# Kernel tuning notes

Hardware: AMD Instinct MI355X
Metric: run time of the kernel (lower is better)

## Reference

```python
import jax, jax.numpy as jnp
import numpy as np

D_MODEL = 768
D_INNER = 1536      # expand=2
D_STATE = 16
DT_RANK = 48        # ceil(768/16)
D_CONV = 4
DEPTH = 24
NUM_CLASSES = 527
GRID = (8, 64)      # (128/16, 1024/16)
SEQ = GRID[0] * GRID[1]
TOKPOS = SEQ // 2   # middle cls token position


def setup_inputs() -> dict:
    key = jax.random.key(0)
    ks = jax.random.split(key, 12)
    rn = lambda k, s, sc=0.02: jax.random.normal(k, s, jnp.float32) * sc
    A_init = jnp.log(jnp.arange(1, D_STATE + 1, dtype=jnp.float32))  # S4D-real init
    return {
        "x": jax.random.normal(ks[0], (1, 1, 128, 1024), jnp.float32),
        "patch_w": rn(ks[1], (D_MODEL, 1, 16, 16)),
        "patch_b": jnp.zeros((D_MODEL,), jnp.float32),
        "cls_token": rn(ks[2], (1, 1, D_MODEL)),
        "pos_embed": rn(ks[3], (1, SEQ + 1, D_MODEL)),
        "in_proj_w": rn(ks[4], (DEPTH, 2 * D_INNER, D_MODEL)),
        "conv_w": rn(ks[5], (DEPTH, 2, D_INNER, D_CONV), 0.1),
        "conv_b": jnp.zeros((DEPTH, 2, D_INNER), jnp.float32),
        "xproj_w": rn(ks[6], (DEPTH, 2, DT_RANK + 2 * D_STATE, D_INNER)),
        "dtproj_w": rn(ks[7], (DEPTH, 2, D_INNER, DT_RANK), 0.1),
        "dtproj_b": jnp.full((DEPTH, 2, D_INNER), float(np.log(np.expm1(0.01))), jnp.float32),
        "A_log": jnp.ones((DEPTH, 2, D_INNER, 1), jnp.float32) * A_init,
        "D_skip": jnp.ones((DEPTH, 2, D_INNER), jnp.float32),
        "out_proj_w": rn(ks[8], (DEPTH, D_MODEL, D_INNER)),
        "norm_w": jnp.ones((DEPTH, D_MODEL), jnp.float32),
        "norm_f_w": jnp.ones((D_MODEL,), jnp.float32),
        "head_w": rn(ks[9], (NUM_CLASSES, D_MODEL)),
        "head_b": jnp.zeros((NUM_CLASSES,), jnp.float32),
    }


def _rmsnorm(x, w, eps=1e-5):
    return x * jax.lax.rsqrt(jnp.mean(x * x, axis=-1, keepdims=True) + eps) * w


def _causal_conv_silu(x, w, b):
    # x [B,d,L], depthwise causal conv, kernel D_CONV, left-pad D_CONV-1
    L = x.shape[-1]
    xp = jnp.pad(x, ((0, 0), (0, 0), (D_CONV - 1, 0)))
    y = sum(w[:, k, None] * xp[:, :, k:k + L] for k in range(D_CONV)) + b[:, None]
    return jax.nn.silu(y)


def _selective_scan(dt, A, Bm, C, u):
    # dt,u: [B,d,L]; Bm,C: [B,N,L]; A: [d,N] (negative)
    def step(h, inp):
        dt_t, B_t, C_t, u_t = inp           # [B,d],[B,N],[B,N],[B,d]
        h = h * jnp.exp(dt_t[..., None] * A) + (dt_t * u_t)[..., None] * B_t[:, None, :]
        return h, jnp.einsum('bdn,bn->bd', h, C_t)
    h0 = jnp.zeros((dt.shape[0], A.shape[0], A.shape[1]), dt.dtype)
    mv = lambda a: jnp.moveaxis(a, -1, 0)
    _, ys = jax.lax.scan(step, h0, (mv(dt), mv(Bm), mv(C), mv(u)))
    return jnp.moveaxis(ys, 0, -1)          # [B,d,L]


def _mamba_dir(x, z, cw, cb, xw, dw, db, A_log, Dsk):
    xc = _causal_conv_silu(x, cw, cb)
    dbl = jnp.einsum('bdl,cd->bcl', xc, xw)                 # [B, R+2N, L]
    dt = jax.nn.softplus(jnp.einsum('brl,dr->bdl', dbl[:, :DT_RANK], dw) + db[:, None])
    Bm = dbl[:, DT_RANK:DT_RANK + D_STATE]
    C = dbl[:, DT_RANK + D_STATE:]
    y = _selective_scan(dt, -jnp.exp(A_log), Bm, C, xc) + Dsk[:, None] * xc
    return y * jax.nn.silu(z)


def _block(carry, p):
    hidden, residual = carry
    ipw, cw, cb, xw, dw, db, A_log, Dsk, opw, nw = p
    residual = residual + hidden                            # add -> norm -> mixer
    h = _rmsnorm(residual, nw)
    xz = jnp.einsum('bld,ed->ble', h, ipw)                  # [B,L,2*d_inner]
    x, z = jnp.split(jnp.moveaxis(xz, -1, 1), 2, axis=1)    # each [B,d_inner,L]
    yf = _mamba_dir(x, z, cw[0], cb[0], xw[0], dw[0], db[0], A_log[0], Dsk[0])
    yb = _mamba_dir(x[:, :, ::-1], z[:, :, ::-1], cw[1], cb[1], xw[1], dw[1],
                    db[1], A_log[1], Dsk[1])[:, :, ::-1]
    out = jnp.einsum('bdl,ed->ble', (yf + yb) * 0.5, opw)   # if_devide_out
    return (out, residual), None


def reference(x, patch_w, patch_b, cls_token, pos_embed, in_proj_w, conv_w, conv_b,
              xproj_w, dtproj_w, dtproj_b, A_log, D_skip, out_proj_w, norm_w,
              norm_f_w, head_w, head_b):
    h = jax.lax.conv_general_dilated(x, patch_w, (16, 16), 'VALID',
                                     dimension_numbers=('NCHW', 'OIHW', 'NCHW'))
    h = h + patch_b[None, :, None, None]
    B = h.shape[0]
    h = h.reshape(B, D_MODEL, SEQ).transpose(0, 2, 1)       # [B,512,768]
    cls = jnp.broadcast_to(cls_token, (B, 1, D_MODEL))
    h = jnp.concatenate([h[:, :TOKPOS], cls, h[:, TOKPOS:]], axis=1)  # [B,513,768]
    h = h + pos_embed
    carry = (h, jnp.zeros_like(h))
    (hidden, residual), _ = jax.lax.scan(
        _block, carry,
        (in_proj_w, conv_w, conv_b, xproj_w, dtproj_w, dtproj_b, A_log, D_skip,
         out_proj_w, norm_w))
    out = _rmsnorm(residual + hidden, norm_f_w)
    feat = out[:, TOKPOS]                                   # middle cls token
    return feat @ head_w.T + head_b
```

## Files before the change

### kernel.cpp

```cpp
#include <hip/hip_runtime.h>

#define L_SEQ 513
#define DM 768
#define DI 1536
#define DSTATE 16
#define DTRANK 48
#define NCLS 527
#define DEPTH 24
#define NC 32
#define CLEN 17

typedef unsigned short u16;
typedef __bf16 bf16x8 __attribute__((ext_vector_type(8)));
typedef float f32x4 __attribute__((ext_vector_type(4)));

#define MFMA_BF16(A, B, C) __builtin_amdgcn_mfma_f32_16x16x32_bf16(A, B, C, 0, 0, 0)

__device__ inline u16 f2bf(float x) {
  unsigned u = __float_as_uint(x);
  return (u16)((u + 0x7FFFu + ((u >> 16) & 1u)) >> 16);
}
__device__ inline float bf2f(u16 h) { return __uint_as_float((unsigned)h << 16); }
__device__ inline void split2(float v, u16& h, u16& l) {
  h = f2bf(v);
  l = f2bf(v - bf2f(h));
}

__global__ void wconvert_kernel(const float* __restrict__ src,
                                u16* __restrict__ hi, u16* __restrict__ lo,
                                long n4) {
  long i = (long)blockIdx.x * 256 + threadIdx.x;
  long stride = (long)gridDim.x * 256;
  for (; i < n4; i += stride) {
    float4 v = ((const float4*)src)[i];
    ushort4 h, l;
    split2(v.x, h.x, l.x);
    split2(v.y, h.y, l.y);
    split2(v.z, h.z, l.z);
    split2(v.w, h.w, l.w);
    ((ushort4*)hi)[i] = h;
    ((ushort4*)lo)[i] = l;
  }
}

__global__ void patch_embed_kernel(const float* __restrict__ x,
                                   const float* __restrict__ pw,
                                   const float* __restrict__ pb,
                                   const float* __restrict__ cls,
                                   const float* __restrict__ pos,
                                   float* __restrict__ hidden,
                                   float* __restrict__ residual) {
  int c = blockIdx.x * 256 + threadIdx.x;
  int s = blockIdx.y;
  if (c >= DM) return;
  float val;
  if (s == 256) {
    val = cls[c];
  } else {
    int p = s - (s > 256 ? 1 : 0);
    int gy = p >> 6, gx = p & 63;
    const float* xp = x + gy * 16 * 1024 + gx * 16;
    const float* wp = pw + c * 256;
    float acc = pb[c];
#pragma unroll 4
    for (int ky = 0; ky < 16; ++ky)
#pragma unroll
      for (int kx = 0; kx < 16; ++kx)
        acc += xp[ky * 1024 + kx] * wp[ky * 16 + kx];
    val = acc;
  }
  long idx = (long)s * DM + c;
  hidden[idx] = val + pos[idx];
  residual[idx] = 0.f;
}

__global__ void rmsnorm_kernel(const float* __restrict__ hidden,
                               float* __restrict__ residual,
                               u16* __restrict__ hnh, u16* __restrict__ hnl,
                               const float* __restrict__ w) {
  int t = blockIdx.x;
  const float* hrow = hidden + (long)t * DM;
  float* rrow = residual + (long)t * DM;
  int tid = threadIdx.x;
  float vals[3];
  float ss = 0.f;
#pragma unroll
  for (int i = 0; i < 3; ++i) {
    int c = tid + i * 256;
    float v = rrow[c] + hrow[c];
    vals[i] = v;
    rrow[c] = v;
    ss += v * v;
  }
#pragma unroll
  for (int o = 32; o; o >>= 1) ss += __shfl_down(ss, o, 64);
  __shared__ float sacc[4];
  if ((tid & 63) == 0) sacc[tid >> 6] = ss;
  __syncthreads();
  float tot = sacc[0] + sacc[1] + sacc[2] + sacc[3];
  float rs = rsqrtf(tot / (float)DM + 1e-5f);
#pragma unroll
  for (int i = 0; i < 3; ++i) {
    int c = tid + i * 256;
    float y = vals[i] * rs * w[c];
    u16 h, l;
    split2(y, h, l);
    hnh[(long)t * DM + c] = h;
    hnl[(long)t * DM + c] = l;
  }
}

__global__ __launch_bounds__(256) void gemm_hl(
    const u16* __restrict__ Ah, const u16* __restrict__ Al,
    const u16* __restrict__ Bh, const u16* __restrict__ Bl,
    float* __restrict__ C,
    int M, int N, int K, int lda, int ldb, int ldc,
    long sA, long sB, long sC,
    const float* __restrict__ bias, long sBias, int act,
    u16* __restrict__ Chi, u16* __restrict__ Clo, int ncap, int ldhl, long sChl) {
  int bz = blockIdx.z;
  const u16* Ahb = Ah + (long)bz * sA;
  const u16* Alb = Al + (long)bz * sA;
  const u16* Bhb = Bh + (long)bz * sB;
  const u16* Blb = Bl + (long)bz * sB;
  float* Cb = C + (long)bz * sC;
  const float* biasb = bias ? bias + (long)bz * sBias : nullptr;

  __shared__ u16 AhS[2][64 * 32], AlS[2][64 * 32];
  __shared__ u16 BhS[2][64 * 32], BlS[2][64 * 32];

  int tid = threadIdx.x;
  int m0 = blockIdx.y * 64, n0 = blockIdx.x * 64;

  int srow = tid >> 2;
  int sg = tid & 3;
  int sIdx = srow * 32 + ((sg ^ ((srow >> 1) & 3)) << 3);
  int arow = m0 + srow, brow = n0 + srow;
  const u16* ah_p = Ahb + (long)arow * lda + sg * 8;
  const u16* al_p = Alb + (long)arow * lda + sg * 8;
  const u16* bh_p = Bhb + (long)brow * ldb + sg * 8;
  const u16* bl_p = Blb + (long)brow * ldb + sg * 8;
  bool aok = arow < M, bok = brow < N;

  int lane = tid & 63;
  int w = tid >> 6;
  int wr = w >> 1, wc = w & 1;
  int fr = lane & 15, kh = lane >> 4;
  int rowA0 = wr * 32 + fr, rowA1 = rowA0 + 16;
  int rowB0 = wc * 32 + fr, rowB1 = rowB0 + 16;
  int offA0 = rowA0 * 32 + ((kh ^ ((rowA0 >> 1) & 3)) << 3);
  int offA1 = rowA1 * 32 + ((kh ^ ((rowA1 >> 1) & 3)) << 3);
  int offB0 = rowB0 * 32 + ((kh ^ ((rowB0 >> 1) & 3)) << 3);
  int offB1 = rowB1 * 32 + ((kh ^ ((rowB1 >> 1) & 3)) << 3);

  f32x4 acc00 = {0.f, 0.f, 0.f, 0.f}, acc01 = {0.f, 0.f, 0.f, 0.f};
  f32x4 acc10 = {0.f, 0.f, 0.f, 0.f}, acc11 = {0.f, 0.f, 0.f, 0.f};

  int nst = (K + 31) / 32;
  int kg = sg * 8;

  uint4 ra, rl_, rb, rbl;
  {
    uint4 z = {0, 0, 0, 0};
    ra = (aok && kg + 8 <= K) ? *(const uint4*)ah_p : z;
    rl_ = (aok && kg + 8 <= K) ? *(const uint4*)al_p : z;
    rb = (bok && kg + 8 <= K) ? *(const uint4*)bh_p : z;
    rbl = (bok && kg + 8 <= K) ? *(const uint4*)bl_p : z;
  }
  *(uint4*)&AhS[0][sIdx] = ra;
  *(uint4*)&AlS[0][sIdx] = rl_;
  *(uint4*)&BhS[0][sIdx] = rb;
  *(uint4*)&BlS[0][sIdx] = rbl;

  for (int s = 0; s < nst; ++s) {
    if (s + 1 < nst) {
      int kb = (s + 1) * 32;
      uint4 z = {0, 0, 0, 0};
      bool kok = kb + kg + 8 <= K;
      ra = (aok && kok) ? *(const uint4*)(ah_p + kb) : z;
      rl_ = (aok && kok) ? *(const uint4*)(al_p + kb) : z;
      rb = (bok && kok) ? *(const uint4*)(bh_p + kb) : z;
      rbl = (bok && kok) ? *(const uint4*)(bl_p + kb) : z;
    }
    __syncthreads();
    int b = s & 1;

    bf16x8 ah0 = __builtin_bit_cast(bf16x8, *(const uint4*)&AhS[b][offA0]);
    bf16x8 ah1 = __builtin_bit_cast(bf16x8, *(const uint4*)&AhS[b][offA1]);
    bf16x8 al0 = __builtin_bit_cast(bf16x8, *(const uint4*)&AlS[b][offA0]);
    bf16x8 al1 = __builtin_bit_cast(bf16x8, *(const uint4*)&AlS[b][offA1]);
    bf16x8 bh0 = __builtin_bit_cast(bf16x8, *(const uint4*)&BhS[b][offB0]);
    bf16x8 bh1 = __builtin_bit_cast(bf16x8, *(const uint4*)&BhS[b][offB1]);
    bf16x8 bl0 = __builtin_bit_cast(bf16x8, *(const uint4*)&BlS[b][offB0]);
    bf16x8 bl1 = __builtin_bit_cast(bf16x8, *(const uint4*)&BlS[b][offB1]);

    acc00 = MFMA_BF16(ah0, bh0, acc00);
    acc00 = MFMA_BF16(ah0, bl0, acc00);
    acc00 = MFMA_BF16(al0, bh0, acc00);
    acc01 = MFMA_BF16(ah0, bh1, acc01);
    acc01 = MFMA_BF16(ah0, bl1, acc01);
    acc01 = MFMA_BF16(al0, bh1, acc01);
    acc10 = MFMA_BF16(ah1, bh0, acc10);
    acc10 = MFMA_BF16(ah1, bl0, acc10);
    acc10 = MFMA_BF16(al1, bh0, acc10);
    acc11 = MFMA_BF16(ah1, bh1, acc11);
    acc11 = MFMA_BF16(ah1, bl1, acc11);
    acc11 = MFMA_BF16(al1, bh1, acc11);

    if (s + 1 < nst) {
      int b2 = (s + 1) & 1;
      *(uint4*)&AhS[b2][sIdx] = ra;
      *(uint4*)&AlS[b2][sIdx] = rl_;
      *(uint4*)&BhS[b2][sIdx] = rb;
      *(uint4*)&BlS[b2][sIdx] = rbl;
    }
  }

  u16* Chib = Chi ? Chi + (long)bz * sChl : nullptr;
  u16* Clob = Clo ? Clo + (long)bz * sChl : nullptr;
  int mbase = m0 + wr * 32, nbase = n0 + wc * 32;
#define WRITE_FRAG(ACC, MI, NI)                                       \
  {                                                                   \
    int n = nbase + (NI)*16 + fr;                                     \
    if (n < N) {                                                      \
      float bv = biasb ? biasb[n] : 0.f;                              \
      _Pragma("unroll")                                               \
      for (int r = 0; r < 4; ++r) {                                   \
        int m = mbase + (MI)*16 + kh * 4 + r;                         \
        if (m < M) {                                                  \
          float v = ACC[r] + bv;                                      \
          if (act == 1) v = (v > 20.f) ? v : log1pf(__expf(v));       \
          Cb[(long)m * ldc + n] = v;                                  \
          if (Chib && n < ncap) {                                     \
            u16 hh, ll;                                               \
            split2(v, hh, ll);                                        \
            Chib[(long)m * ldhl + n] = hh;                            \
            Clob[(long)m * ldhl + n] = ll;                            \
          }                                                           \
        }                                                             \
      }                                                               \
    }                                                                 \
  }
  WRITE_FRAG(acc00, 0, 0)
  WRITE_FRAG(acc01, 0, 1)
  WRITE_FRAG(acc10, 1, 0)
  WRITE_FRAG(acc11, 1, 1)
#undef WRITE_FRAG
}

__global__ void conv_silu_kernel(const float* __restrict__ xz,
                                 const float* __restrict__ cw,
                                 const float* __restrict__ cb,
                                 float* __restrict__ xc,
                                 u16* __restrict__ xch, u16* __restrict__ xcl) {
  int dir = blockIdx.y;
  int idx = blockIdx.x * 256 + threadIdx.x;
  int d = idx % DI;
  int t = idx / DI;
  const float* w = cw + ((long)dir * DI + d) * 4;
  float acc = cb[dir * DI + d];
#pragma unroll
  for (int k = 0; k < 4; ++k) {
    int tau = t + k - 3;
    if (tau >= 0) {
      int tsrc = dir ? (L_SEQ - 1 - tau) : tau;
      acc += w[k] * xz[(long)tsrc * (2 * DI) + d];
    }
  }
  float s = acc / (1.f + __expf(-acc));
  long o = ((long)dir * L_SEQ + t) * DI + d;
  xc[o] = s;
  u16 h, l;
  split2(s, h, l);
  xch[o] = h;
  xcl[o] = l;
}

__global__ __launch_bounds__(256) void scan_part1(
    const float* __restrict__ dtv_arr,
    const float* __restrict__ xc,
    const float* __restrict__ dbl,
    const float* __restrict__ A_log,
    float* __restrict__ part_h,
    float* __restrict__ part_S) {
  int dir = blockIdx.z;
  int c = blockIdx.y;
  int d = blockIdx.x * 256 + threadIdx.x;
  int t0 = c * CLEN;
  int t1 = min(t0 + CLEN, L_SEQ);

  __shared__ float Bs[CLEN][DSTATE];
  const float* dblp = dbl + (long)dir * L_SEQ * 80;
  for (int i = threadIdx.x; i < (t1 - t0) * DSTATE; i += 256) {
    int tt = i >> 4, n = i & 15;
    Bs[tt][n] = dblp[(long)(t0 + tt) * 80 + DTRANK + n];
  }
  __syncthreads();

  float negA[DSTATE], h[DSTATE];
#pragma unroll
  for (int n = 0; n < DSTATE; ++n) {
    negA[n] = -__expf(A_log[((long)dir * DI + d) * DSTATE + n]);
    h[n] = 0.f;
  }
  const float* dtp = dtv_arr + (long)dir * L_SEQ * DI;
  const float* xcp = xc + (long)dir * L_SEQ * DI;

  float S = 0.f;
  float dt_c = 0.f, u_c = 0.f;
  if (t0 < t1) {
    dt_c = dtp[(long)t0 * DI + d];
    u_c = xcp[(long)t0 * DI + d];
  }
  for (int t = t0; t < t1; ++t) {
    float dt_n = 0.f, u_n = 0.f;
    if (t + 1 < t1) {
      dt_n = dtp[(long)(t + 1) * DI + d];
      u_n = xcp[(long)(t + 1) * DI + d];
    }
    S += dt_c;
    float du = dt_c * u_c;
    int tt = t - t0;
#pragma unroll
    for (int n = 0; n < DSTATE; ++n)
      h[n] = h[n] * __expf(dt_c * negA[n]) + du * Bs[tt][n];
    dt_c = dt_n;
    u_c = u_n;
  }
  long base = ((long)dir * NC + c) * DI + d;
  part_S[base] = S;
#pragma unroll
  for (int n = 0; n < DSTATE; ++n) part_h[base * DSTATE + n] = h[n];
}

__global__ void scan_fix(const float* __restrict__ A_log,
                         const float* __restrict__ part_S,
                         float* __restrict__ part_h) {
  int idx = blockIdx.x * 256 + threadIdx.x;
  int n = idx & 15;
  int d = (idx >> 4) % DI;
  int dir = (idx >> 4) / DI;
  float negA = -__expf(A_log[((long)dir * DI + d) * DSTATE + n]);
  float h = 0.f;
  for (int c = 0; c < NC; ++c) {
    long base = ((long)dir * NC + c) * DI + d;
    float S = part_S[base];
    float q = part_h[base * DSTATE + n];
    part_h[base * DSTATE + n] = h;
    h = h * __expf(negA * S) + q;
  }
}

__global__ __launch_bounds__(256) void scan_part2(
    const float* __restrict__ dtv_arr,
    const float* __restrict__ xc,
    const float* __restrict__ dbl,
    const float* __restrict__ xz,
    const float* __restrict__ A_log,
    const float* __restrict__ Dsk,
    const float* __restrict__ part_h,
    float* __restrict__ y) {
  int dir = blockIdx.z;
  int c = blockIdx.y;
  int d = blockIdx.x * 256 + threadIdx.x;
  int t0 = c * CLEN;
  int t1 = min(t0 + CLEN, L_SEQ);

  __shared__ float Bs[CLEN][DSTATE];
  __shared__ float Cs[CLEN][DSTATE];
  const float* dblp = dbl + (long)dir * L_SEQ * 80;
  for (int i = threadIdx.x; i < (t1 - t0) * 2 * DSTATE; i += 256) {
    int tt = i >> 5, j = i & 31;
    float v = dblp[(long)(t0 + tt) * 80 + DTRANK + j];
    if (j < DSTATE) Bs[tt][j] = v; else Cs[tt][j - DSTATE] = v;
  }
  __syncthreads();

  float negA[DSTATE], h[DSTATE];
  long base = ((long)dir * NC + c) * DI + d;
#pragma unroll
  for (int n = 0; n < DSTATE; ++n) {
    negA[n] = -__expf(A_log[((long)dir * DI + d) * DSTATE + n]);
    h[n] = part_h[base * DSTATE + n];
  }
  float dskip = Dsk[dir * DI + d];
  const float* dtp = dtv_arr + (long)dir * L_SEQ * DI;
  const float* xcp = xc + (long)dir * L_SEQ * DI;

  float dt_c = 0.f, u_c = 0.f;
  if (t0 < t1) {
    dt_c = dtp[(long)t0 * DI + d];
    u_c = xcp[(long)t0 * DI + d];
  }
  for (int t = t0; t < t1; ++t) {
    float dt_n = 0.f, u_n = 0.f;
    if (t + 1 < t1) {
      dt_n = dtp[(long)(t + 1) * DI + d];
      u_n = xcp[(long)(t + 1) * DI + d];
    }
    float du = dt_c * u_c;
    int tt = t - t0;
    float acc = 0.f;
#pragma unroll
    for (int n = 0; n < DSTATE; ++n) {
      h[n] = h[n] * __expf(dt_c * negA[n]) + du * Bs[tt][n];
      acc += h[n] * Cs[tt][n];
    }
    int tsrc = dir ? (L_SEQ - 1 - t) : t;
    float zv = xz[(long)tsrc * (2 * DI) + DI + d];
    float sz = zv / (1.f + __expf(-zv));
    y[((long)dir * L_SEQ + tsrc) * DI + d] = (acc + dskip * u_c) * sz;
    dt_c = dt_n;
    u_c = u_n;
  }
}

__global__ void yavg_kernel(const float* __restrict__ yf,
                            const float* __restrict__ yb,
                            u16* __restrict__ yh, u16* __restrict__ yl) {
  long i = (long)blockIdx.x * 256 + threadIdx.x;
  if (i >= (long)L_SEQ * DI / 4) return;
  float4 a = ((const float4*)yf)[i];
  float4 b = ((const float4*)yb)[i];
  ushort4 h, l;
  split2(0.5f * (a.x + b.x), h.x, l.x);
  split2(0.5f * (a.y + b.y), h.y, l.y);
  split2(0.5f * (a.z + b.z), h.z, l.z);
  split2(0.5f * (a.w + b.w), h.w, l.w);
  ((ushort4*)yh)[i] = h;
  ((ushort4*)yl)[i] = l;
}

__global__ void head_kernel(const float* __restrict__ residual,
                            const float* __restrict__ hidden,
                            const float* __restrict__ nfw,
                            const float* __restrict__ hw,
                            const float* __restrict__ hb,
                            float* __restrict__ out) {
  int j = blockIdx.x;
  int tid = threadIdx.x;
  const float* r = residual + (long)256 * DM;
  const float* h = hidden + (long)256 * DM;
  float ss = 0.f, dp = 0.f;
#pragma unroll
  for (int i = 0; i < 3; ++i) {
    int c = tid + i * 256;
    float v = r[c] + h[c];
    ss += v * v;
    dp += v * nfw[c] * hw[(long)j * DM + c];
  }
#pragma unroll
  for (int o = 32; o; o >>= 1) {
    ss += __shfl_down(ss, o, 64);
    dp += __shfl_down(dp, o, 64);
  }
  __shared__ float s1[4], s2[4];
  if ((tid & 63) == 0) {
    s1[tid >> 6] = ss;
    s2[tid >> 6] = dp;
  }
  __syncthreads();
  if (tid == 0) {
    float tot = s1[0] + s1[1] + s1[2] + s1[3];
    float d = s2[0] + s2[1] + s2[2] + s2[3];
    out[j] = d * rsqrtf(tot / (float)DM + 1e-5f) + hb[j];
  }
}

extern "C" void kernel_launch(void* const* d_in, const int* in_sizes, int n_in,
                              void* d_out, int out_size, void* d_ws, size_t ws_size,
                              hipStream_t stream) {
  const float* x        = (const float*)d_in[0];
  const float* patch_w  = (const float*)d_in[1];
  const float* patch_b  = (const float*)d_in[2];
  const float* cls_tok  = (const float*)d_in[3];
  const float* pos_emb  = (const float*)d_in[4];
  const float* in_proj  = (const float*)d_in[5];
  const float* conv_w   = (const float*)d_in[6];
  const float* conv_b   = (const float*)d_in[7];
  const float* xproj_w  = (const float*)d_in[8];
  const float* dtproj_w = (const float*)d_in[9];
  const float* dtproj_b = (const float*)d_in[10];
  const float* A_log    = (const float*)d_in[11];
  const float* D_skip   = (const float*)d_in[12];
  const float* out_proj = (const float*)d_in[13];
  const float* norm_w   = (const float*)d_in[14];
  const float* norm_f_w = (const float*)d_in[15];
  const float* head_w   = (const float*)d_in[16];
  const float* head_b   = (const float*)d_in[17];
  float* out = (float*)d_out;

  float* ws = (float*)d_ws;
  float* residual = ws; ws += (long)L_SEQ * DM;
  float* hidden   = ws; ws += (long)L_SEQ * DM;
  float* xz       = ws; ws += (long)L_SEQ * 2 * DI;
  float* xc       = ws; ws += (long)2 * L_SEQ * DI;
  float* dbl      = ws; ws += (long)2 * L_SEQ * 80;
  float* dtb      = ws; ws += (long)2 * L_SEQ * DI;
  float* yb       = ws; ws += (long)2 * L_SEQ * DI;
  float* part_h   = ws; ws += (long)2 * NC * DI * DSTATE;
  float* part_S   = ws; ws += (long)2 * NC * DI;

  u16* wsu = (u16*)ws;
  const long N_HN  = (long)L_SEQ * DM;
  const long N_XC  = (long)2 * L_SEQ * DI;
  const long N_D48 = (long)2 * L_SEQ * DTRANK;
  const long N_YA  = (long)L_SEQ * DI;
  const long N_WI  = (long)DEPTH * 2 * DI * DM;
  const long N_WX  = (long)DEPTH * 2 * 80 * DI;
  const long N_WD  = (long)DEPTH * 2 * DI * DTRANK;
  const long N_WO  = (long)DEPTH * DM * DI;
  u16* hn_h  = wsu; wsu += N_HN;
  u16* hn_l  = wsu; wsu += N_HN;
  u16* xc_h  = wsu; wsu += N_XC;
  u16* xc_l  = wsu; wsu += N_XC;
  u16* d48_h = wsu; wsu += N_D48;
  u16* d48_l = wsu; wsu += N_D48;
  u16* ya_h  = wsu; wsu += N_YA;
  u16* ya_l  = wsu; wsu += N_YA;
  u16* wi_h  = wsu; wsu += N_WI;
  u16* wi_l  = wsu; wsu += N_WI;
  u16* wx_h  = wsu; wsu += N_WX;
  u16* wx_l  = wsu; wsu += N_WX;
  u16* wd_h  = wsu; wsu += N_WD;
  u16* wd_l  = wsu; wsu += N_WD;
  u16* wo_h  = wsu; wsu += N_WO;
  u16* wo_l  = wsu; wsu += N_WO;

  wconvert_kernel<<<2048, 256, 0, stream>>>(in_proj,  wi_h, wi_l, N_WI / 4);
  wconvert_kernel<<<512,  256, 0, stream>>>(xproj_w,  wx_h, wx_l, N_WX / 4);
  wconvert_kernel<<<512,  256, 0, stream>>>(dtproj_w, wd_h, wd_l, N_WD / 4);
  wconvert_kernel<<<2048, 256, 0, stream>>>(out_proj, wo_h, wo_l, N_WO / 4);

  patch_embed_kernel<<<dim3(3, L_SEQ), 256, 0, stream>>>(
      x, patch_w, patch_b, cls_tok, pos_emb, hidden, residual);

  for (int l = 0; l < DEPTH; ++l) {
    const u16* wih = wi_h + (long)l * 2 * DI * DM;
    const u16* wil = wi_l + (long)l * 2 * DI * DM;
    const u16* wxh = wx_h + (long)l * 2 * 80 * DI;
    const u16* wxl = wx_l + (long)l * 2 * 80 * DI;
    const u16* wdh = wd_h + (long)l * 2 * DI * DTRANK;
    const u16* wdl = wd_l + (long)l * 2 * DI * DTRANK;
    const u16* woh = wo_h + (long)l * DM * DI;
    const u16* wol = wo_l + (long)l * DM * DI;
    const float* cw  = conv_w   + (long)l * 2 * DI * 4;
    const float* cb  = conv_b   + (long)l * 2 * DI;
    const float* db  = dtproj_b + (long)l * 2 * DI;
    const float* Al  = A_log    + (long)l * 2 * DI * DSTATE;
    const float* Dk  = D_skip   + (long)l * 2 * DI;
    const float* nw  = norm_w   + (long)l * DM;

    rmsnorm_kernel<<<L_SEQ, 256, 0, stream>>>(hidden, residual, hn_h, hn_l, nw);

    gemm_hl<<<dim3(48, 9, 1), 256, 0, stream>>>(
        hn_h, hn_l, wih, wil, xz, L_SEQ, 2 * DI, DM, DM, DM, 2 * DI, 0, 0, 0,
        nullptr, 0, 0, nullptr, nullptr, 0, 0, 0);

    conv_silu_kernel<<<dim3(3078, 2), 256, 0, stream>>>(xz, cw, cb, xc, xc_h, xc_l);

    gemm_hl<<<dim3(2, 9, 2), 256, 0, stream>>>(
        xc_h, xc_l, wxh, wxl, dbl, L_SEQ, 80, DI, DI, DI, 80,
        (long)L_SEQ * DI, (long)80 * DI, (long)L_SEQ * 80,
        nullptr, 0, 0, d48_h, d48_l, DTRANK, DTRANK, (long)L_SEQ * DTRANK);

    gemm_hl<<<dim3(24, 9, 2), 256, 0, stream>>>(
        d48_h, d48_l, wdh, wdl, dtb, L_SEQ, DI, DTRANK, DTRANK, DTRANK, DI,
        (long)L_SEQ * DTRANK, (long)DI * DTRANK, (long)L_SEQ * DI,
        db, DI, 1, nullptr, nullptr, 0, 0, 0);

    scan_part1<<<dim3(DI / 256, NC, 2), 256, 0, stream>>>(
        dtb, xc, dbl, Al, part_h, part_S);
    scan_fix<<<(2 * DI * DSTATE) / 256, 256, 0, stream>>>(Al, part_S, part_h);
    scan_part2<<<dim3(DI / 256, NC, 2), 256, 0, stream>>>(
        dtb, xc, dbl, xz, Al, Dk, part_h, yb);

    yavg_kernel<<<(L_SEQ * DI / 4 + 255) / 256, 256, 0, stream>>>(
        yb, yb + (long)L_SEQ * DI, ya_h, ya_l);

    gemm_hl<<<dim3(12, 9, 1), 256, 0, stream>>>(
        ya_h, ya_l, woh, wol, hidden, L_SEQ, DM, DI, DI, DI, DM, 0, 0, 0,
        nullptr, 0, 0, nullptr, nullptr, 0, 0, 0);
  }

  head_kernel<<<NCLS, 256, 0, stream>>>(residual, hidden, norm_f_w, head_w, head_b, out);
}
```

Before: 3.969 ms.

## Use 128x128 split-K GEMM tiles and fuse the three-pass scan into one kernel

Replaces the 64x64 hi/lo bf16 GEMM with a 128x128-tile version that supports split-K. Partial sums are written to separate buffers and reduced by the consumers: rmsnorm, conv_silu, a new xreduce kernel and the head. The chunked selective scan's three kernels (part1, fix, part2) are merged into one block-local kernel that does the chunk carry fix-up in shared memory. This aims to raise MFMA reuse and occupancy on the small-M GEMMs and to cut launch and global round-trip costs for the scan. The cost is extra partial-sum traffic and reduction reads, and fewer threads for the scan's sequential passes.

```diff
diff --git a/kernel.cpp b/kernel.cpp
--- a/kernel.cpp
+++ b/kernel.cpp
@@ -9,6 +9,9 @@
 #define DEPTH 24
 #define NC 32
 #define CLEN 17
+#define SKI 3
+#define SKX 8
+#define SKO 8
 
 typedef unsigned short u16;
 typedef __bf16 bf16x8 __attribute__((ext_vector_type(8)));
@@ -24,6 +27,10 @@
 __device__ inline void split2(float v, u16& h, u16& l) {
   h = f2bf(v);
   l = f2bf(v - bf2f(h));
+}
+__device__ __forceinline__ int lofs(int row, int g) {
+  int swz = (row & 3) ^ ((row >> 2) & 3);
+  return row * 32 + ((g ^ swz) << 3);
 }
 
 __global__ void wconvert_kernel(const float* __restrict__ src,
@@ -74,12 +81,11 @@
   residual[idx] = 0.f;
 }
 
-__global__ void rmsnorm_kernel(const float* __restrict__ hidden,
+__global__ void rmsnorm_kernel(const float* __restrict__ hp, int nparts, long pstr,
                                float* __restrict__ residual,
                                u16* __restrict__ hnh, u16* __restrict__ hnl,
                                const float* __restrict__ w) {
   int t = blockIdx.x;
-  const float* hrow = hidden + (long)t * DM;
   float* rrow = residual + (long)t * DM;
   int tid = threadIdx.x;
   float vals[3];
@@ -87,7 +93,8 @@
 #pragma unroll
   for (int i = 0; i < 3; ++i) {
     int c = tid + i * 256;
-    float v = rrow[c] + hrow[c];
+    float v = rrow[c];
+    for (int p = 0; p < nparts; ++p) v += hp[(long)p * pstr + (long)t * DM + c];
     vals[i] = v;
     rrow[c] = v;
     ss += v * v;
@@ -110,149 +117,132 @@
   }
 }
 
-__global__ __launch_bounds__(256) void gemm_hl(
+#define LOADSTEP(KB)                                                    \
+  {                                                                     \
+    int k_ = (KB) + g0 * 8;                                             \
+    bool kk_ = (k_ + 8 <= kend);                                        \
+    uint4 zz = {0, 0, 0, 0};                                            \
+    a0h = (kk_ && am0) ? *(const uint4*)(Ahb + aoff0 + k_) : zz;        \
+    a1h = (kk_ && am1) ? *(const uint4*)(Ahb + aoff1 + k_) : zz;        \
+    a0l = (kk_ && am0) ? *(const uint4*)(Alb + aoff0 + k_) : zz;        \
+    a1l = (kk_ && am1) ? *(const uint4*)(Alb + aoff1 + k_) : zz;        \
+    b0h = (kk_ && bm0) ? *(const uint4*)(Bhb + boff0 + k_) : zz;        \
+    b1h = (kk_ && bm1) ? *(const uint4*)(Bhb + boff1 + k_) : zz;        \
+    b0l = (kk_ && bm0) ? *(const uint4*)(Blb + boff0 + k_) : zz;        \
+    b1l = (kk_ && bm1) ? *(const uint4*)(Blb + boff1 + k_) : zz;        \
+  }
+#define WRITEBUF(B)                        \
+  {                                        \
+    *(uint4*)&SA[B][0][l0] = a0h;          \
+    *(uint4*)&SA[B][0][l1] = a1h;          \
+    *(uint4*)&SA[B][1][l0] = a0l;          \
+    *(uint4*)&SA[B][1][l1] = a1l;          \
+    *(uint4*)&SB[B][0][l0] = b0h;          \
+    *(uint4*)&SB[B][0][l1] = b1h;          \
+    *(uint4*)&SB[B][1][l0] = b0l;          \
+    *(uint4*)&SB[B][1][l1] = b1l;          \
+  }
+
+__global__ __launch_bounds__(256) void gemm128(
     const u16* __restrict__ Ah, const u16* __restrict__ Al,
     const u16* __restrict__ Bh, const u16* __restrict__ Bl,
     float* __restrict__ C,
     int M, int N, int K, int lda, int ldb, int ldc,
     long sA, long sB, long sC,
-    const float* __restrict__ bias, long sBias, int act,
-    u16* __restrict__ Chi, u16* __restrict__ Clo, int ncap, int ldhl, long sChl) {
-  int bz = blockIdx.z;
-  const u16* Ahb = Ah + (long)bz * sA;
-  const u16* Alb = Al + (long)bz * sA;
-  const u16* Bhb = Bh + (long)bz * sB;
-  const u16* Blb = Bl + (long)bz * sB;
-  float* Cb = C + (long)bz * sC;
-  const float* biasb = bias ? bias + (long)bz * sBias : nullptr;
-
-  __shared__ u16 AhS[2][64 * 32], AlS[2][64 * 32];
-  __shared__ u16 BhS[2][64 * 32], BlS[2][64 * 32];
+    int NSK, int Kb, long sP,
+    const float* __restrict__ bias, long sBias, int act) {
+  int z = blockIdx.z;
+  int batch = z / NSK, sk = z - batch * NSK;
+  const u16* Ahb = Ah + (long)batch * sA;
+  const u16* Alb = Al + (long)batch * sA;
+  const u16* Bhb = Bh + (long)batch * sB;
+  const u16* Blb = Bl + (long)batch * sB;
+  float* Cb = C + (long)batch * sC + (long)sk * sP;
+  const float* biasb = bias ? bias + (long)batch * sBias : nullptr;
+  int ks0 = sk * Kb;
+  int kend = min(ks0 + Kb, K);
+
+  __shared__ u16 SA[2][2][128 * 32];
+  __shared__ u16 SB[2][2][128 * 32];
 
   int tid = threadIdx.x;
-  int m0 = blockIdx.y * 64, n0 = blockIdx.x * 64;
-
-  int srow = tid >> 2;
-  int sg = tid & 3;
-  int sIdx = srow * 32 + ((sg ^ ((srow >> 1) & 3)) << 3);
-  int arow = m0 + srow, brow = n0 + srow;
-  const u16* ah_p = Ahb + (long)arow * lda + sg * 8;
-  const u16* al_p = Alb + (long)arow * lda + sg * 8;
-  const u16* bh_p = Bhb + (long)brow * ldb + sg * 8;
-  const u16* bl_p = Blb + (long)brow * ldb + sg * 8;
-  bool aok = arow < M, bok = brow < N;
-
-  int lane = tid & 63;
-  int w = tid >> 6;
+  int m0 = blockIdx.y * 128, n0 = blockIdx.x * 128;
+
+  int r0 = tid >> 2, g0 = tid & 3;
+  int r1 = r0 + 64;
+  int l0 = lofs(r0, g0), l1 = lofs(r1, g0);
+  long aoff0 = (long)(m0 + r0) * lda, aoff1 = (long)(m0 + r1) * lda;
+  long boff0 = (long)(n0 + r0) * ldb, boff1 = (long)(n0 + r1) * ldb;
+  bool am0 = (m0 + r0) < M, am1 = (m0 + r1) < M;
+  bool bm0 = (n0 + r0) < N, bm1 = (n0 + r1) < N;
+
+  int lane = tid & 63, w = tid >> 6;
   int wr = w >> 1, wc = w & 1;
   int fr = lane & 15, kh = lane >> 4;
-  int rowA0 = wr * 32 + fr, rowA1 = rowA0 + 16;
-  int rowB0 = wc * 32 + fr, rowB1 = rowB0 + 16;
-  int offA0 = rowA0 * 32 + ((kh ^ ((rowA0 >> 1) & 3)) << 3);
-  int offA1 = rowA1 * 32 + ((kh ^ ((rowA1 >> 1) & 3)) << 3);
-  int offB0 = rowB0 * 32 + ((kh ^ ((rowB0 >> 1) & 3)) << 3);
-  int offB1 = rowB1 * 32 + ((kh ^ ((rowB1 >> 1) & 3)) << 3);
-
-  f32x4 acc00 = {0.f, 0.f, 0.f, 0.f}, acc01 = {0.f, 0.f, 0.f, 0.f};
-  f32x4 acc10 = {0.f, 0.f, 0.f, 0.f}, acc11 = {0.f, 0.f, 0.f, 0.f};
-
-  int nst = (K + 31) / 32;
-  int kg = sg * 8;
-
-  uint4 ra, rl_, rb, rbl;
-  {
-    uint4 z = {0, 0, 0, 0};
-    ra = (aok && kg + 8 <= K) ? *(const uint4*)ah_p : z;
-    rl_ = (aok && kg + 8 <= K) ? *(const uint4*)al_p : z;
-    rb = (bok && kg + 8 <= K) ? *(const uint4*)bh_p : z;
-    rbl = (bok && kg + 8 <= K) ? *(const uint4*)bl_p : z;
-  }
-  *(uint4*)&AhS[0][sIdx] = ra;
-  *(uint4*)&AlS[0][sIdx] = rl_;
-  *(uint4*)&BhS[0][sIdx] = rb;
-  *(uint4*)&BlS[0][sIdx] = rbl;
+  int offA[4], offB[4];
+#pragma unroll
+  for (int i = 0; i < 4; ++i) {
+    offA[i] = lofs(wr * 64 + i * 16 + fr, kh);
+    offB[i] = lofs(wc * 64 + i * 16 + fr, kh);
+  }
+
+  f32x4 acc[4][4] = {};
+  int nst = (kend - ks0 + 31) >> 5;
+  uint4 a0h, a1h, a0l, a1l, b0h, b1h, b0l, b1l;
+  LOADSTEP(ks0);
+  WRITEBUF(0);
+  if (nst > 1) LOADSTEP(ks0 + 32);
+  __syncthreads();
 
   for (int s = 0; s < nst; ++s) {
+    int b = s & 1;
+    bf16x8 fah[4], fal[4], fbh[4], fbl[4];
+#pragma unroll
+    for (int i = 0; i < 4; ++i) {
+      fah[i] = __builtin_bit_cast(bf16x8, *(const uint4*)&SA[b][0][offA[i]]);
+      fal[i] = __builtin_bit_cast(bf16x8, *(const uint4*)&SA[b][1][offA[i]]);
+      fbh[i] = __builtin_bit_cast(bf16x8, *(const uint4*)&SB[b][0][offB[i]]);
+      fbl[i] = __builtin_bit_cast(bf16x8, *(const uint4*)&SB[b][1][offB[i]]);
+    }
+#pragma unroll
+    for (int mi = 0; mi < 4; ++mi)
+#pragma unroll
+      for (int ni = 0; ni < 4; ++ni) {
+        acc[mi][ni] = MFMA_BF16(fah[mi], fbh[ni], acc[mi][ni]);
+        acc[mi][ni] = MFMA_BF16(fah[mi], fbl[ni], acc[mi][ni]);
+        acc[mi][ni] = MFMA_BF16(fal[mi], fbh[ni], acc[mi][ni]);
+      }
     if (s + 1 < nst) {
-      int kb = (s + 1) * 32;
-      uint4 z = {0, 0, 0, 0};
-      bool kok = kb + kg + 8 <= K;
-      ra = (aok && kok) ? *(const uint4*)(ah_p + kb) : z;
-      rl_ = (aok && kok) ? *(const uint4*)(al_p + kb) : z;
-      rb = (bok && kok) ? *(const uint4*)(bh_p + kb) : z;
-      rbl = (bok && kok) ? *(const uint4*)(bl_p + kb) : z;
+      WRITEBUF(b ^ 1);
+      if (s + 2 < nst) LOADSTEP(ks0 + (s + 2) * 32);
     }
     __syncthreads();
-    int b = s & 1;
-
-    bf16x8 ah0 = __builtin_bit_cast(bf16x8, *(const uint4*)&AhS[b][offA0]);
-    bf16x8 ah1 = __builtin_bit_cast(bf16x8, *(const uint4*)&AhS[b][offA1]);
-    bf16x8 al0 = __builtin_bit_cast(bf16x8, *(const uint4*)&AlS[b][offA0]);
-    bf16x8 al1 = __builtin_bit_cast(bf16x8, *(const uint4*)&AlS[b][offA1]);
-    bf16x8 bh0 = __builtin_bit_cast(bf16x8, *(const uint4*)&BhS[b][offB0]);
-    bf16x8 bh1 = __builtin_bit_cast(bf16x8, *(const uint4*)&BhS[b][offB1]);
-    bf16x8 bl0 = __builtin_bit_cast(bf16x8, *(const uint4*)&BlS[b][offB0]);
-    bf16x8 bl1 = __builtin_bit_cast(bf16x8, *(const uint4*)&BlS[b][offB1]);
-
-    acc00 = MFMA_BF16(ah0, bh0, acc00);
-    acc00 = MFMA_BF16(ah0, bl0, acc00);
-    acc00 = MFMA_BF16(al0, bh0, acc00);
-    acc01 = MFMA_BF16(ah0, bh1, acc01);
-    acc01 = MFMA_BF16(ah0, bl1, acc01);
-    acc01 = MFMA_BF16(al0, bh1, acc01);
-    acc10 = MFMA_BF16(ah1, bh0, acc10);
-    acc10 = MFMA_BF16(ah1, bl0, acc10);
-    acc10 = MFMA_BF16(al1, bh0, acc10);
-    acc11 = MFMA_BF16(ah1, bh1, acc11);
-    acc11 = MFMA_BF16(ah1, bl1, acc11);
-    acc11 = MFMA_BF16(al1, bh1, acc11);
-
-    if (s + 1 < nst) {
-      int b2 = (s + 1) & 1;
-      *(uint4*)&AhS[b2][sIdx] = ra;
-      *(uint4*)&AlS[b2][sIdx] = rl_;
-      *(uint4*)&BhS[b2][sIdx] = rb;
-      *(uint4*)&BlS[b2][sIdx] = rbl;
-    }
-  }
-
-  u16* Chib = Chi ? Chi + (long)bz * sChl : nullptr;
-  u16* Clob = Clo ? Clo + (long)bz * sChl : nullptr;
-  int mbase = m0 + wr * 32, nbase = n0 + wc * 32;
-#define WRITE_FRAG(ACC, MI, NI)                                       \
-  {                                                                   \
-    int n = nbase + (NI)*16 + fr;                                     \
-    if (n < N) {                                                      \
-      float bv = biasb ? biasb[n] : 0.f;                              \
-      _Pragma("unroll")                                               \
-      for (int r = 0; r < 4; ++r) {                                   \
-        int m = mbase + (MI)*16 + kh * 4 + r;                         \
-        if (m < M) {                                                  \
-          float v = ACC[r] + bv;                                      \
-          if (act == 1) v = (v > 20.f) ? v : log1pf(__expf(v));       \
-          Cb[(long)m * ldc + n] = v;                                  \
-          if (Chib && n < ncap) {                                     \
-            u16 hh, ll;                                               \
-            split2(v, hh, ll);                                        \
-            Chib[(long)m * ldhl + n] = hh;                            \
-            Clob[(long)m * ldhl + n] = ll;                            \
-          }                                                           \
-        }                                                             \
-      }                                                               \
-    }                                                                 \
-  }
-  WRITE_FRAG(acc00, 0, 0)
-  WRITE_FRAG(acc01, 0, 1)
-  WRITE_FRAG(acc10, 1, 0)
-  WRITE_FRAG(acc11, 1, 1)
-#undef WRITE_FRAG
-}
-
-__global__ void conv_silu_kernel(const float* __restrict__ xz,
+  }
+
+#pragma unroll
+  for (int mi = 0; mi < 4; ++mi)
+#pragma unroll
+    for (int ni = 0; ni < 4; ++ni) {
+      int n = n0 + wc * 64 + ni * 16 + fr;
+      if (n >= N) continue;
+      float bv = biasb ? biasb[n] : 0.f;
+#pragma unroll
+      for (int r = 0; r < 4; ++r) {
+        int m = m0 + wr * 64 + mi * 16 + kh * 4 + r;
+        if (m >= M) continue;
+        float v = acc[mi][ni][r] + bv;
+        if (act == 1) v = (v > 20.f) ? v : log1pf(__expf(v));
+        Cb[(long)m * ldc + n] = v;
+      }
+    }
+}
+
+__global__ void conv_silu_kernel(const float* __restrict__ xz_p,
                                  const float* __restrict__ cw,
                                  const float* __restrict__ cb,
                                  float* __restrict__ xc,
                                  u16* __restrict__ xch, u16* __restrict__ xcl) {
+  const long PZ = (long)L_SEQ * 2 * DI;
   int dir = blockIdx.y;
   int idx = blockIdx.x * 256 + threadIdx.x;
   int d = idx % DI;
@@ -264,7 +254,9 @@
     int tau = t + k - 3;
     if (tau >= 0) {
       int tsrc = dir ? (L_SEQ - 1 - tau) : tau;
-      acc += w[k] * xz[(long)tsrc * (2 * DI) + d];
+      long o = (long)tsrc * (2 * DI) + d;
+      float xv = xz_p[o] + xz_p[o + PZ] + xz_p[o + 2 * PZ];
+      acc += w[k] * xv;
     }
   }
   float s = acc / (1.f + __expf(-acc));
@@ -276,142 +268,120 @@
   xcl[o] = l;
 }
 
-__global__ __launch_bounds__(256) void scan_part1(
+__global__ void xreduce_kernel(const float* __restrict__ dbl_p,
+                               float* __restrict__ dbl,
+                               u16* __restrict__ d48h, u16* __restrict__ d48l) {
+  int idx = blockIdx.x * 256 + threadIdx.x;
+  if (idx >= 2 * L_SEQ * 80) return;
+  int j = idx % 80;
+  int td = idx / 80;
+  int dir = td / L_SEQ;
+  int t = td - dir * L_SEQ;
+  const float* p = dbl_p + (long)dir * SKX * L_SEQ * 80 + (long)t * 80 + j;
+  float v = 0.f;
+#pragma unroll
+  for (int q = 0; q < SKX; ++q) v += p[(long)q * L_SEQ * 80];
+  dbl[((long)dir * L_SEQ + t) * 80 + j] = v;
+  if (j < DTRANK) {
+    u16 h, l;
+    split2(v, h, l);
+    long o = ((long)dir * L_SEQ + t) * DTRANK + j;
+    d48h[o] = h;
+    d48l[o] = l;
+  }
+}
+
+__global__ __launch_bounds__(256) void scan_all(
     const float* __restrict__ dtv_arr,
     const float* __restrict__ xc,
     const float* __restrict__ dbl,
+    const float* __restrict__ xz_p,
     const float* __restrict__ A_log,
-    float* __restrict__ part_h,
-    float* __restrict__ part_S) {
-  int dir = blockIdx.z;
-  int c = blockIdx.y;
-  int d = blockIdx.x * 256 + threadIdx.x;
-  int t0 = c * CLEN;
-  int t1 = min(t0 + CLEN, L_SEQ);
-
-  __shared__ float Bs[CLEN][DSTATE];
-  const float* dblp = dbl + (long)dir * L_SEQ * 80;
-  for (int i = threadIdx.x; i < (t1 - t0) * DSTATE; i += 256) {
-    int tt = i >> 4, n = i & 15;
-    Bs[tt][n] = dblp[(long)(t0 + tt) * 80 + DTRANK + n];
-  }
-  __syncthreads();
-
-  float negA[DSTATE], h[DSTATE];
-#pragma unroll
-  for (int n = 0; n < DSTATE; ++n) {
-    negA[n] = -__expf(A_log[((long)dir * DI + d) * DSTATE + n]);
-    h[n] = 0.f;
-  }
+    const float* __restrict__ Dsk,
+    float* __restrict__ y) {
+  const long PZ = (long)L_SEQ * 2 * DI;
+  int dir = blockIdx.y;
+  int d0 = blockIdx.x * 8;
+  int tid = threadIdx.x;
+  __shared__ float Q[8][NC][DSTATE];
+  __shared__ float Sv[8][NC];
+
   const float* dtp = dtv_arr + (long)dir * L_SEQ * DI;
   const float* xcp = xc + (long)dir * L_SEQ * DI;
-
-  float S = 0.f;
-  float dt_c = 0.f, u_c = 0.f;
-  if (t0 < t1) {
-    dt_c = dtp[(long)t0 * DI + d];
-    u_c = xcp[(long)t0 * DI + d];
-  }
-  for (int t = t0; t < t1; ++t) {
-    float dt_n = 0.f, u_n = 0.f;
-    if (t + 1 < t1) {
-      dt_n = dtp[(long)(t + 1) * DI + d];
-      u_n = xcp[(long)(t + 1) * DI + d];
-    }
-    S += dt_c;
-    float du = dt_c * u_c;
-    int tt = t - t0;
-#pragma unroll
-    for (int n = 0; n < DSTATE; ++n)
-      h[n] = h[n] * __expf(dt_c * negA[n]) + du * Bs[tt][n];
-    dt_c = dt_n;
-    u_c = u_n;
-  }
-  long base = ((long)dir * NC + c) * DI + d;
-  part_S[base] = S;
-#pragma unroll
-  for (int n = 0; n < DSTATE; ++n) part_h[base * DSTATE + n] = h[n];
-}
-
-__global__ void scan_fix(const float* __restrict__ A_log,
-                         const float* __restrict__ part_S,
-                         float* __restrict__ part_h) {
-  int idx = blockIdx.x * 256 + threadIdx.x;
-  int n = idx & 15;
-  int d = (idx >> 4) % DI;
-  int dir = (idx >> 4) / DI;
-  float negA = -__expf(A_log[((long)dir * DI + d) * DSTATE + n]);
-  float h = 0.f;
-  for (int c = 0; c < NC; ++c) {
-    long base = ((long)dir * NC + c) * DI + d;
-    float S = part_S[base];
-    float q = part_h[base * DSTATE + n];
-    part_h[base * DSTATE + n] = h;
-    h = h * __expf(negA * S) + q;
-  }
-}
-
-__global__ __launch_bounds__(256) void scan_part2(
-    const float* __restrict__ dtv_arr,
-    const float* __restrict__ xc,
-    const float* __restrict__ dbl,
-    const float* __restrict__ xz,
-    const float* __restrict__ A_log,
-    const float* __restrict__ Dsk,
-    const float* __restrict__ part_h,
-    float* __restrict__ y) {
-  int dir = blockIdx.z;
-  int c = blockIdx.y;
-  int d = blockIdx.x * 256 + threadIdx.x;
-  int t0 = c * CLEN;
-  int t1 = min(t0 + CLEN, L_SEQ);
-
-  __shared__ float Bs[CLEN][DSTATE];
-  __shared__ float Cs[CLEN][DSTATE];
   const float* dblp = dbl + (long)dir * L_SEQ * 80;
-  for (int i = threadIdx.x; i < (t1 - t0) * 2 * DSTATE; i += 256) {
-    int tt = i >> 5, j = i & 31;
-    float v = dblp[(long)(t0 + tt) * 80 + DTRANK + j];
-    if (j < DSTATE) Bs[tt][j] = v; else Cs[tt][j - DSTATE] = v;
+
+  int dl = tid & 7, c = tid >> 3;
+  int d = d0 + dl;
+  float negA[DSTATE];
+#pragma unroll
+  for (int n = 0; n < DSTATE; ++n)
+    negA[n] = -__expf(A_log[((long)dir * DI + d) * DSTATE + n]);
+
+  int t0 = c * CLEN, t1 = min(t0 + CLEN, L_SEQ);
+  {
+    float h[DSTATE];
+#pragma unroll
+    for (int n = 0; n < DSTATE; ++n) h[n] = 0.f;
+    float S = 0.f;
+    for (int t = t0; t < t1; ++t) {
+      float dt = dtp[(long)t * DI + d];
+      float u = xcp[(long)t * DI + d];
+      float du = dt * u;
+      S += dt;
+      const float4* B4 = (const float4*)(dblp + (long)t * 80 + DTRANK);
+      float4 b0 = B4[0], b1 = B4[1], b2 = B4[2], b3 = B4[3];
+      float Bv[DSTATE] = {b0.x, b0.y, b0.z, b0.w, b1.x, b1.y, b1.z, b1.w,
+                          b2.x, b2.y, b2.z, b2.w, b3.x, b3.y, b3.z, b3.w};
+#pragma unroll
+      for (int n = 0; n < DSTATE; ++n)
+        h[n] = h[n] * __expf(dt * negA[n]) + du * Bv[n];
+    }
+    Sv[dl][c] = S;
+#pragma unroll
+    for (int n = 0; n < DSTATE; ++n) Q[dl][c][n] = h[n];
   }
   __syncthreads();
-
-  float negA[DSTATE], h[DSTATE];
-  long base = ((long)dir * NC + c) * DI + d;
-#pragma unroll
-  for (int n = 0; n < DSTATE; ++n) {
-    negA[n] = -__expf(A_log[((long)dir * DI + d) * DSTATE + n]);
-    h[n] = part_h[base * DSTATE + n];
-  }
-  float dskip = Dsk[dir * DI + d];
-  const float* dtp = dtv_arr + (long)dir * L_SEQ * DI;
-  const float* xcp = xc + (long)dir * L_SEQ * DI;
-
-  float dt_c = 0.f, u_c = 0.f;
-  if (t0 < t1) {
-    dt_c = dtp[(long)t0 * DI + d];
-    u_c = xcp[(long)t0 * DI + d];
-  }
-  for (int t = t0; t < t1; ++t) {
-    float dt_n = 0.f, u_n = 0.f;
-    if (t + 1 < t1) {
-      dt_n = dtp[(long)(t + 1) * DI + d];
-      u_n = xcp[(long)(t + 1) * DI + d];
-    }
-    float du = dt_c * u_c;
-    int tt = t - t0;
-    float acc = 0.f;
-#pragma unroll
-    for (int n = 0; n < DSTATE; ++n) {
-      h[n] = h[n] * __expf(dt_c * negA[n]) + du * Bs[tt][n];
-      acc += h[n] * Cs[tt][n];
-    }
-    int tsrc = dir ? (L_SEQ - 1 - t) : t;
-    float zv = xz[(long)tsrc * (2 * DI) + DI + d];
-    float sz = zv / (1.f + __expf(-zv));
-    y[((long)dir * L_SEQ + tsrc) * DI + d] = (acc + dskip * u_c) * sz;
-    dt_c = dt_n;
-    u_c = u_n;
+  if (tid < 128) {
+    int fdl = tid >> 4, n = tid & 15;
+    int fd = d0 + fdl;
+    float nA = -__expf(A_log[((long)dir * DI + fd) * DSTATE + n]);
+    float h = 0.f;
+    for (int cc = 0; cc < NC; ++cc) {
+      float S = Sv[fdl][cc];
+      float q = Q[fdl][cc][n];
+      Q[fdl][cc][n] = h;
+      h = h * __expf(nA * S) + q;
+    }
+  }
+  __syncthreads();
+  {
+    float h[DSTATE];
+#pragma unroll
+    for (int n = 0; n < DSTATE; ++n) h[n] = Q[dl][c][n];
+    float dskip = Dsk[dir * DI + d];
+    for (int t = t0; t < t1; ++t) {
+      float dt = dtp[(long)t * DI + d];
+      float u = xcp[(long)t * DI + d];
+      float du = dt * u;
+      const float4* B4 = (const float4*)(dblp + (long)t * 80 + DTRANK);
+      float4 b0 = B4[0], b1 = B4[1], b2 = B4[2], b3 = B4[3];
+      float4 c0 = B4[4], c1 = B4[5], c2 = B4[6], c3 = B4[7];
+      float Bv[DSTATE] = {b0.x, b0.y, b0.z, b0.w, b1.x, b1.y, b1.z, b1.w,
+                          b2.x, b2.y, b2.z, b2.w, b3.x, b3.y, b3.z, b3.w};
+      float Cv[DSTATE] = {c0.x, c0.y, c0.z, c0.w, c1.x, c1.y, c1.z, c1.w,
+                          c2.x, c2.y, c2.z, c2.w, c3.x, c3.y, c3.z, c3.w};
+      float acc = 0.f;
+#pragma unroll
+      for (int n = 0; n < DSTATE; ++n) {
+        h[n] = h[n] * __expf(dt * negA[n]) + du * Bv[n];
+        acc += h[n] * Cv[n];
+      }
+      int tsrc = dir ? (L_SEQ - 1 - t) : t;
+      long zo = (long)tsrc * (2 * DI) + DI + d;
+      float zv = xz_p[zo] + xz_p[zo + PZ] + xz_p[zo + 2 * PZ];
+      float sz = zv / (1.f + __expf(-zv));
+      y[((long)dir * L_SEQ + tsrc) * DI + d] = (acc + dskip * u) * sz;
+    }
   }
 }
 
@@ -432,7 +402,7 @@
 }
 
 __global__ void head_kernel(const float* __restrict__ residual,
-                            const float* __restrict__ hidden,
+                            const float* __restrict__ hp, long pstr,
                             const float* __restrict__ nfw,
                             const float* __restrict__ hw,
                             const float* __restrict__ hb,
@@ -440,12 +410,12 @@
   int j = blockIdx.x;
   int tid = threadIdx.x;
   const float* r = residual + (long)256 * DM;
-  const float* h = hidden + (long)256 * DM;
   float ss = 0.f, dp = 0.f;
 #pragma unroll
   for (int i = 0; i < 3; ++i) {
     int c = tid + i * 256;
-    float v = r[c] + h[c];
+    float v = r[c];
+    for (int p = 0; p < SKO; ++p) v += hp[(long)p * pstr + (long)256 * DM + c];
     ss += v * v;
     dp += v * nfw[c] * hw[(long)j * DM + c];
   }
@@ -490,19 +460,21 @@
   const float* head_b   = (const float*)d_in[17];
   float* out = (float*)d_out;
 
+  const long PHN = (long)L_SEQ * DM;
+  const long PZ  = (long)L_SEQ * 2 * DI;
+
   float* ws = (float*)d_ws;
-  float* residual = ws; ws += (long)L_SEQ * DM;
-  float* hidden   = ws; ws += (long)L_SEQ * DM;
-  float* xz       = ws; ws += (long)L_SEQ * 2 * DI;
+  float* residual = ws; ws += PHN;
+  float* xz_p     = ws; ws += SKI * PZ;
   float* xc       = ws; ws += (long)2 * L_SEQ * DI;
   float* dbl      = ws; ws += (long)2 * L_SEQ * 80;
+  float* dbl_p    = ws; ws += (long)2 * SKX * L_SEQ * 80;
   float* dtb      = ws; ws += (long)2 * L_SEQ * DI;
   float* yb       = ws; ws += (long)2 * L_SEQ * DI;
-  float* part_h   = ws; ws += (long)2 * NC * DI * DSTATE;
-  float* part_S   = ws; ws += (long)2 * NC * DI;
+  float* hid_p    = ws; ws += (long)SKO * PHN;
 
   u16* wsu = (u16*)ws;
-  const long N_HN  = (long)L_SEQ * DM;
+  const long N_HN  = PHN;
   const long N_XC  = (long)2 * L_SEQ * DI;
   const long N_D48 = (long)2 * L_SEQ * DTRANK;
   const long N_YA  = (long)L_SEQ * DI;
@@ -533,7 +505,7 @@
   wconvert_kernel<<<2048, 256, 0, stream>>>(out_proj, wo_h, wo_l, N_WO / 4);
 
   patch_embed_kernel<<<dim3(3, L_SEQ), 256, 0, stream>>>(
-      x, patch_w, patch_b, cls_tok, pos_emb, hidden, residual);
+      x, patch_w, patch_b, cls_tok, pos_emb, hid_p, residual);
 
   for (int l = 0; l < DEPTH; ++l) {
     const u16* wih = wi_h + (long)l * 2 * DI * DM;
@@ -551,37 +523,39 @@
     const float* Dk  = D_skip   + (long)l * 2 * DI;
     const float* nw  = norm_w   + (long)l * DM;
 
-    rmsnorm_kernel<<<L_SEQ, 256, 0, stream>>>(hidden, residual, hn_h, hn_l, nw);
-
-    gemm_hl<<<dim3(48, 9, 1), 256, 0, stream>>>(
-        hn_h, hn_l, wih, wil, xz, L_SEQ, 2 * DI, DM, DM, DM, 2 * DI, 0, 0, 0,
-        nullptr, 0, 0, nullptr, nullptr, 0, 0, 0);
-
-    conv_silu_kernel<<<dim3(3078, 2), 256, 0, stream>>>(xz, cw, cb, xc, xc_h, xc_l);
-
-    gemm_hl<<<dim3(2, 9, 2), 256, 0, stream>>>(
-        xc_h, xc_l, wxh, wxl, dbl, L_SEQ, 80, DI, DI, DI, 80,
-        (long)L_SEQ * DI, (long)80 * DI, (long)L_SEQ * 80,
-        nullptr, 0, 0, d48_h, d48_l, DTRANK, DTRANK, (long)L_SEQ * DTRANK);
-
-    gemm_hl<<<dim3(24, 9, 2), 256, 0, stream>>>(
+    rmsnorm_kernel<<<L_SEQ, 256, 0, stream>>>(
+        hid_p, (l == 0) ? 1 : SKO, PHN, residual, hn_h, hn_l, nw);
+
+    gemm128<<<dim3(24, 5, SKI), 256, 0, stream>>>(
+        hn_h, hn_l, wih, wil, xz_p, L_SEQ, 2 * DI, DM, DM, DM, 2 * DI,
+        0, 0, 0, SKI, DM / SKI, PZ, nullptr, 0, 0);
+
+    conv_silu_kernel<<<dim3(3078, 2), 256, 0, stream>>>(xz_p, cw, cb, xc, xc_h, xc_l);
+
+    gemm128<<<dim3(1, 5, 2 * SKX), 256, 0, stream>>>(
+        xc_h, xc_l, wxh, wxl, dbl_p, L_SEQ, 80, DI, DI, DI, 80,
+        (long)L_SEQ * DI, (long)80 * DI, (long)SKX * L_SEQ * 80,
+        SKX, DI / SKX, (long)L_SEQ * 80, nullptr, 0, 0);
+
+    xreduce_kernel<<<(2 * L_SEQ * 80 + 255) / 256, 256, 0, stream>>>(
+        dbl_p, dbl, d48_h, d48_l);
+
+    gemm128<<<dim3(12, 5, 2), 256, 0, stream>>>(
         d48_h, d48_l, wdh, wdl, dtb, L_SEQ, DI, DTRANK, DTRANK, DTRANK, DI,
         (long)L_SEQ * DTRANK, (long)DI * DTRANK, (long)L_SEQ * DI,
-        db, DI, 1, nullptr, nullptr, 0, 0, 0);
-
-    scan_part1<<<dim3(DI / 256, NC, 2), 256, 0, stream>>>(
-        dtb, xc, dbl, Al, part_h, part_S);
-    scan_fix<<<(2 * DI * DSTATE) / 256, 256, 0, stream>>>(Al, part_S, part_h);
-    scan_part2<<<dim3(DI / 256, NC, 2), 256, 0, stream>>>(
-        dtb, xc, dbl, xz, Al, Dk, part_h, yb);
+        1, DTRANK, 0, db, DI, 1);
+
+    scan_all<<<dim3(DI / 8, 2), 256, 0, stream>>>(
+        dtb, xc, dbl, xz_p, Al, Dk, yb);
 
     yavg_kernel<<<(L_SEQ * DI / 4 + 255) / 256, 256, 0, stream>>>(
         yb, yb + (long)L_SEQ * DI, ya_h, ya_l);
 
-    gemm_hl<<<dim3(12, 9, 1), 256, 0, stream>>>(
-        ya_h, ya_l, woh, wol, hidden, L_SEQ, DM, DI, DI, DI, DM, 0, 0, 0,
-        nullptr, 0, 0, nullptr, nullptr, 0, 0, 0);
-  }
-
-  head_kernel<<<NCLS, 256, 0, stream>>>(residual, hidden, norm_f_w, head_w, head_b, out);
-}
+    gemm128<<<dim3(6, 5, SKO), 256, 0, stream>>>(
+        ya_h, ya_l, woh, wol, hid_p, L_SEQ, DM, DI, DI, DI, DM,
+        0, 0, 0, SKO, DI / SKO, PHN, nullptr, 0, 0);
+  }
+
+  head_kernel<<<NCLS, 256, 0, stream>>>(residual, hid_p, PHN,
+                                        norm_f_w, head_w, head_b, out);
+}
```

Measured after the change: 4.010 ms. About the same (+1.0%).
